# Optimization experiments

Hardware: AMD Instinct MI355X
Metric: run time of the kernel (lower is better)

Reference implementation:

```python
import jax, jax.numpy as jnp
import numpy as np

H = 4096      # hidden_size (Llama-7B)
I = 11008     # intermediate_size (Llama-7B)
T = 4096      # tokens = batch 2 * seq 2048


def setup_inputs() -> dict:
    key = jax.random.key(0)
    ks = jax.random.split(key, 10)
    # int8 activations in [-128, 127]
    x = jax.random.randint(ks[0], (T, H), -128, 128, dtype=jnp.int32).astype(jnp.int8)
    # int4 weights stored as int8 values in [-8, 7], layout [out, in]
    gate_w = jax.random.randint(ks[1], (I, H), -8, 8, dtype=jnp.int32).astype(jnp.int8)
    up_w   = jax.random.randint(ks[2], (I, H), -8, 8, dtype=jnp.int32).astype(jnp.int8)
    down_w = jax.random.randint(ks[3], (H, I), -8, 8, dtype=jnp.int32).astype(jnp.int8)
    # per-output-channel dequant scale (input_scale * weight_scale) and fp32 bias
    gate_alpha = jax.random.uniform(ks[4], (I,), jnp.float32, 1e-4, 3e-4)
    up_alpha   = jax.random.uniform(ks[5], (I,), jnp.float32, 1e-4, 3e-4)
    down_alpha = jax.random.uniform(ks[6], (H,), jnp.float32, 1e-4, 3e-4)
    gate_bias = jax.random.normal(ks[7], (I,), jnp.float32) * 0.01
    up_bias   = jax.random.normal(ks[8], (I,), jnp.float32) * 0.01
    down_bias = jax.random.normal(ks[9], (H,), jnp.float32) * 0.01
    down_input_scale = jnp.array(0.1, dtype=jnp.float32)
    return dict(x=x, gate_w=gate_w, up_w=up_w, down_w=down_w,
                gate_alpha=gate_alpha, gate_bias=gate_bias,
                up_alpha=up_alpha, up_bias=up_bias,
                down_alpha=down_alpha, down_bias=down_bias,
                down_input_scale=down_input_scale)


def _w4a8_linear(x_i8, w_i4, alpha, bias):
    # int8 act x int4 weight -> int32 accumulate, per-out-channel dequant, fp32 out
    acc = jnp.matmul(x_i8.astype(jnp.int32), w_i4.T.astype(jnp.int32))  # [T, out]
    return acc.astype(jnp.float32) * alpha + bias


def reference(x, gate_w, up_w, down_w, gate_alpha, gate_bias, up_alpha, up_bias,
              down_alpha, down_bias, down_input_scale):
    g = _w4a8_linear(x, gate_w, gate_alpha, gate_bias)          # [T, I] fp32
    u = _w4a8_linear(x, up_w, up_alpha, up_bias)                # [T, I] fp32
    h = jax.nn.silu(g) * u                                      # SwiGLU
    # requantize to int8 for down_proj input (values kept exact as fp32)
    hq = jnp.clip(jnp.round(h / down_input_scale), -128.0, 127.0)
    out = jnp.matmul(hq, down_w.T.astype(jnp.float32)) * down_alpha + down_bias
    return out
```

## Files before the change

kernel.cpp:

```cpp
#include <hip/hip_runtime.h>
#include <stdint.h>

#define H_DIM 4096
#define I_DIM 11008
#define T_DIM 4096

typedef int i32x4 __attribute__((ext_vector_type(4)));
typedef const void __attribute__((address_space(1))) gvoid_t;
typedef void __attribute__((address_space(3))) svoid_t;

__device__ __forceinline__ void gload_lds16(const void* gsrc, void* ldst) {
    __builtin_amdgcn_global_load_lds((gvoid_t*)gsrc, (svoid_t*)ldst, 16, 0, 0);
}
__device__ __forceinline__ void wait_vmcnt8() {
    asm volatile("s_waitcnt vmcnt(8)" ::: "memory");
}
__device__ __forceinline__ void wait_vmcnt0() {
    asm volatile("s_waitcnt vmcnt(0)" ::: "memory");
}
__device__ __forceinline__ void wait_lgkm0() {
    asm volatile("s_waitcnt lgkmcnt(0)" ::: "memory");
    __builtin_amdgcn_sched_barrier(0);
}
__device__ __forceinline__ void barrier_() {
    asm volatile("s_barrier" ::: "memory");
}

__device__ __forceinline__ uint32_t pack4(int4 v) {
    uint32_t r = (uint32_t)(uint8_t)v.x;
    r |= (uint32_t)(uint8_t)v.y << 8;
    r |= (uint32_t)(uint8_t)v.z << 16;
    r |= (uint32_t)(uint8_t)v.w << 24;
    return r;
}

__global__ void convert_kernel(const int* __restrict__ src, int8_t* __restrict__ dst,
                               int n4) {
    int idx = blockIdx.x * blockDim.x + threadIdx.x;
    int stride = gridDim.x * blockDim.x;
    for (int i = idx; i < n4; i += stride) {
        int4 v = ((const int4*)src)[i];
        ((uint32_t*)dst)[i] = pack4(v);
    }
}

__global__ void convert_frag_kernel(const int* __restrict__ src, int8_t* __restrict__ dst,
                                    int nslots, int kdiv16) {
    const int K = kdiv16 << 4;
    int idx = blockIdx.x * blockDim.x + threadIdx.x;
    int stride = gridDim.x * blockDim.x;
    for (int s = idx; s < nslots; s += stride) {
        const int n_lo = s & 15;
        const int srem = s >> 4;
        const int ks = srem % kdiv16;
        const int nb = srem / kdiv16;
        const int4* p = (const int4*)(src + (size_t)(nb * 16 + n_lo) * K + ks * 16);
        uint4 w;
        w.x = pack4(p[0]); w.y = pack4(p[1]); w.z = pack4(p[2]); w.w = pack4(p[3]);
        const size_t doff = ((size_t)nb * (kdiv16 >> 2) + (ks >> 2)) * 1024
                          + (size_t)(ks & 3) * 256 + (size_t)n_lo * 16;
        *(uint4*)(dst + doff) = w;
    }
}

#define MFMA_I8 __builtin_amdgcn_mfma_i32_16x16x64_i8

__global__ __launch_bounds__(512, 4)
void gateup_kernel(const int8_t* __restrict__ x8, const int8_t* __restrict__ gwf,
                   const int8_t* __restrict__ uwf,
                   const float* __restrict__ galpha, const float* __restrict__ gbias,
                   const float* __restrict__ ualpha, const float* __restrict__ ubias,
                   const float* __restrict__ scale_p, int8_t* __restrict__ hq)
{
    __shared__ __align__(16) int8_t smem_s[65536];

    const int bid = blockIdx.x;
    const int mt = bid & 31;
    const int nt = bid >> 5;
    const int m0 = mt << 7;
    const int n0 = nt << 7;

    const int tid  = threadIdx.x;
    const int lane = tid & 63;
    const int wid  = tid >> 6;
    const int isU  = wid >> 2;
    const int w4   = wid & 3;
    const int wr   = w4 >> 1;
    const int wc   = w4 & 1;
    const int lr   = lane & 15;
    const int rdsw = ((lane >> 4) ^ ((lr >> 1) & 3)) << 4;

    const int srow = tid >> 2;
    const int scol = ((tid & 3) ^ ((tid >> 3) & 3)) << 4;
    const int woff = wid << 10;

    const int8_t* As = x8 + (size_t)(m0 + srow) * H_DIM + scol;
    const int KB64 = H_DIM >> 6;
    const int8_t* Bsel = isU ? uwf : gwf;
    const int8_t* Bq = Bsel + ((size_t)((n0 >> 4) + wc * 4) * KB64) * 1024 + lane * 16;

    i32x4 acc[4][4];
#pragma unroll
    for (int mf = 0; mf < 4; ++mf)
#pragma unroll
        for (int nf = 0; nf < 4; ++nf) acc[mf][nf] = i32x4{0, 0, 0, 0};

    const int aro = (wr * 64 + lr) * 64 + rdsw;

#define STAGE_CH(b, ch) do { \
        _Pragma("unroll") for (int i_ = 0; i_ < 4; ++i_) \
            gload_lds16(As + (ch) * 256 + i_ * 64, \
                        smem_s + (b) * 32768 + i_ * 8192 + woff); \
    } while (0)

#define BLOAD(BF, tt) do { \
        _Pragma("unroll") for (int nf = 0; nf < 4; ++nf) \
            BF[nf] = *(const i32x4*)(Bq + ((size_t)nf * KB64 + (tt)) * 1024); \
    } while (0)

#define INNER(i_, BF, BFN, c_) do { \
        i32x4 af[4]; \
        _Pragma("unroll") for (int mf = 0; mf < 4; ++mf) \
            af[mf] = *(const i32x4*)(smem_s + ((c_) & 1) * 32768 + (i_) * 8192 \
                                     + aro + mf * 1024); \
        BLOAD(BFN, ((c_) * 4 + (i_) + 1) & (NKT - 1)); \
        __builtin_amdgcn_s_setprio(1); \
        _Pragma("unroll") for (int mf = 0; mf < 4; ++mf) \
        _Pragma("unroll") for (int nf = 0; nf < 4; ++nf) \
            acc[mf][nf] = MFMA_I8(af[mf], BF[nf], acc[mf][nf], 0, 0, 0); \
        __builtin_amdgcn_s_setprio(0); \
    } while (0)

    const int NKT = H_DIM / 64;
    const int NC  = NKT / 4;
    i32x4 bfA[4], bfB[4];
    STAGE_CH(0, 0);
    STAGE_CH(1, 1);
    BLOAD(bfA, 0);

    for (int c = 0; c < NC; ++c) {
        wait_vmcnt8();
        barrier_();
        INNER(0, bfA, bfB, c);
        INNER(1, bfB, bfA, c);
        INNER(2, bfA, bfB, c);
        INNER(3, bfB, bfA, c);
        wait_lgkm0();
        barrier_();
        STAGE_CH(c & 1, (c + 2) & (NC - 1));
    }
#undef INNER
#undef BLOAD
#undef STAGE_CH
    wait_vmcnt0();
    barrier_();

    const float scale = *scale_p;
#pragma unroll
    for (int h = 0; h < 2; ++h) {
        if (isU) {
#pragma unroll
            for (int mf = 0; mf < 4; ++mf)
#pragma unroll
                for (int q = 0; q < 2; ++q)
                    *(i32x4*)(smem_s + w4 * 8192 + mf * 2048 + q * 1024 + lane * 16)
                        = acc[mf][h * 2 + q];
        }
        barrier_();
        if (!isU) {
#pragma unroll
            for (int q = 0; q < 2; ++q) {
                const int nf = h * 2 + q;
                const int col = n0 + wc * 64 + nf * 16 + lr;
                const float gA = galpha[col], gB = gbias[col];
                const float uA = ualpha[col], uB = ubias[col];
#pragma unroll
                for (int mf = 0; mf < 4; ++mf) {
                    i32x4 uacc = *(const i32x4*)(smem_s + w4 * 8192 + mf * 2048
                                                 + q * 1024 + lane * 16);
                    const int row0 = m0 + wr * 64 + mf * 16 + (lane >> 4) * 4;
#pragma unroll
                    for (int j = 0; j < 4; ++j) {
                        float g = (float)acc[mf][nf][j] * gA + gB;
                        float u = (float)uacc[j] * uA + uB;
                        float s = 1.0f / (1.0f + __expf(-g));
                        float hh = g * s * u;
                        float qv = rintf(hh / scale);
                        qv = fminf(127.0f, fmaxf(-128.0f, qv));
                        hq[(size_t)(row0 + j) * I_DIM + col] = (int8_t)qv;
                    }
                }
            }
        }
        barrier_();
    }
}

__global__ __launch_bounds__(512, 4)
void down_kernel(const int8_t* __restrict__ hq, const int8_t* __restrict__ dwf,
                 const float* __restrict__ dalpha, const float* __restrict__ dbias,
                 float* __restrict__ out)
{
    __shared__ __align__(16) int8_t smem_d[65536];

    const int bid = blockIdx.x;
    const int mt = bid & 31;
    const int nt = bid >> 5;
    const int m0 = mt << 7;
    const int n0 = nt << 8;

    const int tid  = threadIdx.x;
    const int lane = tid & 63;
    const int wid  = tid >> 6;
    const int wr   = wid >> 2;
    const int wc   = wid & 3;
    const int lr   = lane & 15;
    const int rdsw = ((lane >> 4) ^ ((lr >> 1) & 3)) << 4;

    const int srow = tid >> 2;
    const int scol = ((tid & 3) ^ ((tid >> 3) & 3)) << 4;
    const int woff = wid << 10;

    const int8_t* Ap = hq + (size_t)(m0 + srow) * I_DIM + scol;
    const int KB64 = I_DIM >> 6;
    const int8_t* Bq = dwf + ((size_t)((n0 >> 4) + wc * 4) * KB64) * 1024 + lane * 16;

    i32x4 acc[4][4];
#pragma unroll
    for (int mf = 0; mf < 4; ++mf)
#pragma unroll
        for (int nf = 0; nf < 4; ++nf) acc[mf][nf] = i32x4{0, 0, 0, 0};

    const int aro = (wr * 64 + lr) * 64 + rdsw;

#define STAGE_CH(b, ch) do { \
        _Pragma("unroll") for (int i_ = 0; i_ < 4; ++i_) \
            gload_lds16(Ap + (size_t)(ch) * 256 + i_ * 64, \
                        smem_d + (b) * 32768 + i_ * 8192 + woff); \
    } while (0)

#define BLOAD(BF, tt) do { \
        _Pragma("unroll") for (int nf = 0; nf < 4; ++nf) \
            BF[nf] = *(const i32x4*)(Bq + ((size_t)nf * KB64 + (tt)) * 1024); \
    } while (0)

#define INNER(i_, BF, BFN, c_) do { \
        i32x4 af[4]; \
        _Pragma("unroll") for (int mf = 0; mf < 4; ++mf) \
            af[mf] = *(const i32x4*)(smem_d + ((c_) & 1) * 32768 + (i_) * 8192 \
                                     + aro + mf * 1024); \
        BLOAD(BFN, ((c_) * 4 + (i_) + 1) % NKT); \
        __builtin_amdgcn_s_setprio(1); \
        _Pragma("unroll") for (int mf = 0; mf < 4; ++mf) \
        _Pragma("unroll") for (int nf = 0; nf < 4; ++nf) \
            acc[mf][nf] = MFMA_I8(af[mf], BF[nf], acc[mf][nf], 0, 0, 0); \
        __builtin_amdgcn_s_setprio(0); \
    } while (0)

    const int NKT = I_DIM / 64;
    const int NC  = NKT / 4;
    i32x4 bfA[4], bfB[4];
    STAGE_CH(0, 0);
    STAGE_CH(1, 1);
    BLOAD(bfA, 0);

    for (int c = 0; c < NC; ++c) {
        wait_vmcnt8();
        barrier_();
        INNER(0, bfA, bfB, c);
        INNER(1, bfB, bfA, c);
        INNER(2, bfA, bfB, c);
        INNER(3, bfB, bfA, c);
        wait_lgkm0();
        barrier_();
        STAGE_CH(c & 1, (c + 2) % NC);
    }
#undef INNER
#undef BLOAD
#undef STAGE_CH
    wait_vmcnt0();

#pragma unroll
    for (int nf = 0; nf < 4; ++nf) {
        const int col = n0 + wc * 64 + nf * 16 + lr;
        const float dA = dalpha[col], dB = dbias[col];
#pragma unroll
        for (int mf = 0; mf < 4; ++mf) {
            const int row0 = m0 + wr * 64 + mf * 16 + (lane >> 4) * 4;
#pragma unroll
            for (int j = 0; j < 4; ++j) {
                out[(size_t)(row0 + j) * H_DIM + col] = (float)acc[mf][nf][j] * dA + dB;
            }
        }
    }
}

extern "C" void kernel_launch(void* const* d_in, const int* in_sizes, int n_in,
                              void* d_out, int out_size, void* d_ws, size_t ws_size,
                              hipStream_t stream) {
    const int* x32  = (const int*)d_in[0];
    const int* gw32 = (const int*)d_in[1];
    const int* uw32 = (const int*)d_in[2];
    const int* dw32 = (const int*)d_in[3];
    const float* ga = (const float*)d_in[4];
    const float* gb = (const float*)d_in[5];
    const float* ua = (const float*)d_in[6];
    const float* ub = (const float*)d_in[7];
    const float* da = (const float*)d_in[8];
    const float* db = (const float*)d_in[9];
    const float* sc = (const float*)d_in[10];
    float* out = (float*)d_out;

    const size_t SZ_X8 = (size_t)T_DIM * H_DIM;
    const size_t SZ_W  = (size_t)I_DIM * H_DIM;
    const size_t SZ_HQ = (size_t)T_DIM * I_DIM;

    int8_t* gwf = (int8_t*)d_ws;
    int8_t* uwf = gwf + SZ_W;
    int8_t* hq  = uwf + SZ_W;
    int8_t* x8  = hq + SZ_HQ;

    convert_kernel<<<dim3(2048), dim3(256), 0, stream>>>(x32, x8, (int)(SZ_X8 / 4));
    convert_frag_kernel<<<dim3(2048), dim3(256), 0, stream>>>(
        gw32, gwf, (int)(SZ_W / 16), H_DIM / 16);
    convert_frag_kernel<<<dim3(2048), dim3(256), 0, stream>>>(
        uw32, uwf, (int)(SZ_W / 16), H_DIM / 16);
    gateup_kernel<<<dim3(32 * 86), dim3(512), 0, stream>>>(
        x8, gwf, uwf, ga, gb, ua, ub, sc, hq);
    int8_t* dwf = gwf;
    convert_frag_kernel<<<dim3(2048), dim3(256), 0, stream>>>(
        dw32, dwf, (int)(SZ_W / 16), I_DIM / 16);
    down_kernel<<<dim3(32 * 16), dim3(512), 0, stream>>>(hq, dwf, da, db, out);
}
```

Before: 677.5 us.

## Reshape per-warp tiles to 128x32 so B fragments are loaded once per warp

Each warp's output tile changes from 64x64 (4x4 MFMA fragments) to a full-height 128x32 strip (8x2 fragments) in both the gate/up and down kernels. Every warp now reads all 128 A rows from LDS but loads only two B fragments directly from global memory, which halves per-warp global B traffic and removes the duplicate B loads between row-warps. The cost is double the LDS A reads per warp. The vmcnt wait threshold and the epilogue indexing are adjusted to match the new fragment layout.

```diff
diff --git a/kernel.cpp b/kernel.cpp
--- a/kernel.cpp
+++ b/kernel.cpp
@@ -12,8 +12,8 @@
 __device__ __forceinline__ void gload_lds16(const void* gsrc, void* ldst) {
     __builtin_amdgcn_global_load_lds((gvoid_t*)gsrc, (svoid_t*)ldst, 16, 0, 0);
 }
-__device__ __forceinline__ void wait_vmcnt8() {
-    asm volatile("s_waitcnt vmcnt(8)" ::: "memory");
+__device__ __forceinline__ void wait_vmcnt6() {
+    asm volatile("s_waitcnt vmcnt(6)" ::: "memory");
 }
 __device__ __forceinline__ void wait_vmcnt0() {
     asm volatile("s_waitcnt vmcnt(0)" ::: "memory");
@@ -85,8 +85,6 @@
     const int wid  = tid >> 6;
     const int isU  = wid >> 2;
     const int w4   = wid & 3;
-    const int wr   = w4 >> 1;
-    const int wc   = w4 & 1;
     const int lr   = lane & 15;
     const int rdsw = ((lane >> 4) ^ ((lr >> 1) & 3)) << 4;
 
@@ -97,15 +95,15 @@
     const int8_t* As = x8 + (size_t)(m0 + srow) * H_DIM + scol;
     const int KB64 = H_DIM >> 6;
     const int8_t* Bsel = isU ? uwf : gwf;
-    const int8_t* Bq = Bsel + ((size_t)((n0 >> 4) + wc * 4) * KB64) * 1024 + lane * 16;
-
-    i32x4 acc[4][4];
-#pragma unroll
-    for (int mf = 0; mf < 4; ++mf)
-#pragma unroll
-        for (int nf = 0; nf < 4; ++nf) acc[mf][nf] = i32x4{0, 0, 0, 0};
-
-    const int aro = (wr * 64 + lr) * 64 + rdsw;
+    const int8_t* Bq = Bsel + ((size_t)((n0 >> 4) + w4 * 2) * KB64) * 1024 + lane * 16;
+
+    i32x4 acc[8][2];
+#pragma unroll
+    for (int mf = 0; mf < 8; ++mf)
+#pragma unroll
+        for (int nf = 0; nf < 2; ++nf) acc[mf][nf] = i32x4{0, 0, 0, 0};
+
+    const int aro = lr * 64 + rdsw;
 
 #define STAGE_CH(b, ch) do { \
         _Pragma("unroll") for (int i_ = 0; i_ < 4; ++i_) \
@@ -114,32 +112,32 @@
     } while (0)
 
 #define BLOAD(BF, tt) do { \
-        _Pragma("unroll") for (int nf = 0; nf < 4; ++nf) \
+        _Pragma("unroll") for (int nf = 0; nf < 2; ++nf) \
             BF[nf] = *(const i32x4*)(Bq + ((size_t)nf * KB64 + (tt)) * 1024); \
     } while (0)
 
 #define INNER(i_, BF, BFN, c_) do { \
-        i32x4 af[4]; \
-        _Pragma("unroll") for (int mf = 0; mf < 4; ++mf) \
+        i32x4 af[8]; \
+        _Pragma("unroll") for (int mf = 0; mf < 8; ++mf) \
             af[mf] = *(const i32x4*)(smem_s + ((c_) & 1) * 32768 + (i_) * 8192 \
                                      + aro + mf * 1024); \
         BLOAD(BFN, ((c_) * 4 + (i_) + 1) & (NKT - 1)); \
         __builtin_amdgcn_s_setprio(1); \
-        _Pragma("unroll") for (int mf = 0; mf < 4; ++mf) \
-        _Pragma("unroll") for (int nf = 0; nf < 4; ++nf) \
+        _Pragma("unroll") for (int mf = 0; mf < 8; ++mf) \
+        _Pragma("unroll") for (int nf = 0; nf < 2; ++nf) \
             acc[mf][nf] = MFMA_I8(af[mf], BF[nf], acc[mf][nf], 0, 0, 0); \
         __builtin_amdgcn_s_setprio(0); \
     } while (0)
 
     const int NKT = H_DIM / 64;
     const int NC  = NKT / 4;
-    i32x4 bfA[4], bfB[4];
+    i32x4 bfA[2], bfB[2];
     STAGE_CH(0, 0);
     STAGE_CH(1, 1);
     BLOAD(bfA, 0);
 
     for (int c = 0; c < NC; ++c) {
-        wait_vmcnt8();
+        wait_vmcnt6();
         barrier_();
         INNER(0, bfA, bfB, c);
         INNER(1, bfB, bfA, c);
@@ -160,28 +158,27 @@
     for (int h = 0; h < 2; ++h) {
         if (isU) {
 #pragma unroll
-            for (int mf = 0; mf < 4; ++mf)
-#pragma unroll
-                for (int q = 0; q < 2; ++q)
-                    *(i32x4*)(smem_s + w4 * 8192 + mf * 2048 + q * 1024 + lane * 16)
-                        = acc[mf][h * 2 + q];
+            for (int mq = 0; mq < 4; ++mq)
+#pragma unroll
+                for (int nf = 0; nf < 2; ++nf)
+                    *(i32x4*)(smem_s + w4 * 8192 + mq * 2048 + nf * 1024 + lane * 16)
+                        = acc[h * 4 + mq][nf];
         }
         barrier_();
         if (!isU) {
 #pragma unroll
-            for (int q = 0; q < 2; ++q) {
-                const int nf = h * 2 + q;
-                const int col = n0 + wc * 64 + nf * 16 + lr;
+            for (int nf = 0; nf < 2; ++nf) {
+                const int col = n0 + w4 * 32 + nf * 16 + lr;
                 const float gA = galpha[col], gB = gbias[col];
                 const float uA = ualpha[col], uB = ubias[col];
 #pragma unroll
-                for (int mf = 0; mf < 4; ++mf) {
-                    i32x4 uacc = *(const i32x4*)(smem_s + w4 * 8192 + mf * 2048
-                                                 + q * 1024 + lane * 16);
-                    const int row0 = m0 + wr * 64 + mf * 16 + (lane >> 4) * 4;
+                for (int mq = 0; mq < 4; ++mq) {
+                    i32x4 uacc = *(const i32x4*)(smem_s + w4 * 8192 + mq * 2048
+                                                 + nf * 1024 + lane * 16);
+                    const int row0 = m0 + (h * 4 + mq) * 16 + (lane >> 4) * 4;
 #pragma unroll
                     for (int j = 0; j < 4; ++j) {
-                        float g = (float)acc[mf][nf][j] * gA + gB;
+                        float g = (float)acc[h * 4 + mq][nf][j] * gA + gB;
                         float u = (float)uacc[j] * uA + uB;
                         float s = 1.0f / (1.0f + __expf(-g));
                         float hh = g * s * u;
@@ -212,8 +209,6 @@
     const int tid  = threadIdx.x;
     const int lane = tid & 63;
     const int wid  = tid >> 6;
-    const int wr   = wid >> 2;
-    const int wc   = wid & 3;
     const int lr   = lane & 15;
     const int rdsw = ((lane >> 4) ^ ((lr >> 1) & 3)) << 4;
 
@@ -223,15 +218,15 @@
 
     const int8_t* Ap = hq + (size_t)(m0 + srow) * I_DIM + scol;
     const int KB64 = I_DIM >> 6;
-    const int8_t* Bq = dwf + ((size_t)((n0 >> 4) + wc * 4) * KB64) * 1024 + lane * 16;
-
-    i32x4 acc[4][4];
-#pragma unroll
-    for (int mf = 0; mf < 4; ++mf)
-#pragma unroll
-        for (int nf = 0; nf < 4; ++nf) acc[mf][nf] = i32x4{0, 0, 0, 0};
-
-    const int aro = (wr * 64 + lr) * 64 + rdsw;
+    const int8_t* Bq = dwf + ((size_t)((n0 >> 4) + wid * 2) * KB64) * 1024 + lane * 16;
+
+    i32x4 acc[8][2];
+#pragma unroll
+    for (int mf = 0; mf < 8; ++mf)
+#pragma unroll
+        for (int nf = 0; nf < 2; ++nf) acc[mf][nf] = i32x4{0, 0, 0, 0};
+
+    const int aro = lr * 64 + rdsw;
 
 #define STAGE_CH(b, ch) do { \
         _Pragma("unroll") for (int i_ = 0; i_ < 4; ++i_) \
@@ -240,32 +235,32 @@
     } while (0)
 
 #define BLOAD(BF, tt) do { \
-        _Pragma("unroll") for (int nf = 0; nf < 4; ++nf) \
+        _Pragma("unroll") for (int nf = 0; nf < 2; ++nf) \
             BF[nf] = *(const i32x4*)(Bq + ((size_t)nf * KB64 + (tt)) * 1024); \
     } while (0)
 
 #define INNER(i_, BF, BFN, c_) do { \
-        i32x4 af[4]; \
-        _Pragma("unroll") for (int mf = 0; mf < 4; ++mf) \
+        i32x4 af[8]; \
+        _Pragma("unroll") for (int mf = 0; mf < 8; ++mf) \
             af[mf] = *(const i32x4*)(smem_d + ((c_) & 1) * 32768 + (i_) * 8192 \
                                      + aro + mf * 1024); \
         BLOAD(BFN, ((c_) * 4 + (i_) + 1) % NKT); \
         __builtin_amdgcn_s_setprio(1); \
-        _Pragma("unroll") for (int mf = 0; mf < 4; ++mf) \
-        _Pragma("unroll") for (int nf = 0; nf < 4; ++nf) \
+        _Pragma("unroll") for (int mf = 0; mf < 8; ++mf) \
+        _Pragma("unroll") for (int nf = 0; nf < 2; ++nf) \
             acc[mf][nf] = MFMA_I8(af[mf], BF[nf], acc[mf][nf], 0, 0, 0); \
         __builtin_amdgcn_s_setprio(0); \
     } while (0)
 
     const int NKT = I_DIM / 64;
     const int NC  = NKT / 4;
-    i32x4 bfA[4], bfB[4];
+    i32x4 bfA[2], bfB[2];
     STAGE_CH(0, 0);
     STAGE_CH(1, 1);
     BLOAD(bfA, 0);
 
     for (int c = 0; c < NC; ++c) {
-        wait_vmcnt8();
+        wait_vmcnt6();
         barrier_();
         INNER(0, bfA, bfB, c);
         INNER(1, bfB, bfA, c);
@@ -281,12 +276,12 @@
     wait_vmcnt0();
 
 #pragma unroll
-    for (int nf = 0; nf < 4; ++nf) {
-        const int col = n0 + wc * 64 + nf * 16 + lr;
+    for (int nf = 0; nf < 2; ++nf) {
+        const int col = n0 + wid * 32 + nf * 16 + lr;
         const float dA = dalpha[col], dB = dbias[col];
 #pragma unroll
-        for (int mf = 0; mf < 4; ++mf) {
-            const int row0 = m0 + wr * 64 + mf * 16 + (lane >> 4) * 4;
+        for (int mf = 0; mf < 8; ++mf) {
+            const int row0 = m0 + mf * 16 + (lane >> 4) * 4;
 #pragma unroll
             for (int j = 0; j < 4; ++j) {
                 out[(size_t)(row0 + j) * H_DIM + col] = (float)acc[mf][nf][j] * dA + dB;
```

Result: faster. 639.6 us (-5.6%).

## Halve block threads and double per-warp tile in gate-up and down GEMMs

Applied to the files above, without the earlier changes.

Both GEMM kernels drop from 512 to 256 threads per block, so each wave computes a larger output tile. In gateup, every wave now holds both gate and up accumulators, which removes the LDS exchange and barriers in the SwiGLU epilogue and reuses each A fragment for two MFMAs. In down, each wave covers 8 column fragments instead of 4. This doubles accumulator registers per wave and lowers the number of waves per CU, trading occupancy and latency hiding for more register-level data reuse.

```diff
diff --git a/kernel.cpp b/kernel.cpp
--- a/kernel.cpp
+++ b/kernel.cpp
@@ -12,8 +12,8 @@
 __device__ __forceinline__ void gload_lds16(const void* gsrc, void* ldst) {
     __builtin_amdgcn_global_load_lds((gvoid_t*)gsrc, (svoid_t*)ldst, 16, 0, 0);
 }
-__device__ __forceinline__ void wait_vmcnt8() {
-    asm volatile("s_waitcnt vmcnt(8)" ::: "memory");
+__device__ __forceinline__ void wait_vmcnt16() {
+    asm volatile("s_waitcnt vmcnt(16)" ::: "memory");
 }
 __device__ __forceinline__ void wait_vmcnt0() {
     asm volatile("s_waitcnt vmcnt(0)" ::: "memory");
@@ -65,7 +65,7 @@
 
 #define MFMA_I8 __builtin_amdgcn_mfma_i32_16x16x64_i8
 
-__global__ __launch_bounds__(512, 4)
+__global__ __launch_bounds__(256, 2)
 void gateup_kernel(const int8_t* __restrict__ x8, const int8_t* __restrict__ gwf,
                    const int8_t* __restrict__ uwf,
                    const float* __restrict__ galpha, const float* __restrict__ gbias,
@@ -83,10 +83,8 @@
     const int tid  = threadIdx.x;
     const int lane = tid & 63;
     const int wid  = tid >> 6;
-    const int isU  = wid >> 2;
-    const int w4   = wid & 3;
-    const int wr   = w4 >> 1;
-    const int wc   = w4 & 1;
+    const int wrr  = wid >> 1;
+    const int wcc  = wid & 1;
     const int lr   = lane & 15;
     const int rdsw = ((lane >> 4) ^ ((lr >> 1) & 3)) << 4;
 
@@ -96,55 +94,65 @@
 
     const int8_t* As = x8 + (size_t)(m0 + srow) * H_DIM + scol;
     const int KB64 = H_DIM >> 6;
-    const int8_t* Bsel = isU ? uwf : gwf;
-    const int8_t* Bq = Bsel + ((size_t)((n0 >> 4) + wc * 4) * KB64) * 1024 + lane * 16;
-
-    i32x4 acc[4][4];
+    const int8_t* BqG = gwf + ((size_t)((n0 >> 4) + wcc * 4) * KB64) * 1024 + lane * 16;
+    const int8_t* BqU = uwf + ((size_t)((n0 >> 4) + wcc * 4) * KB64) * 1024 + lane * 16;
+
+    i32x4 accg[4][4], accu[4][4];
 #pragma unroll
     for (int mf = 0; mf < 4; ++mf)
 #pragma unroll
-        for (int nf = 0; nf < 4; ++nf) acc[mf][nf] = i32x4{0, 0, 0, 0};
-
-    const int aro = (wr * 64 + lr) * 64 + rdsw;
+        for (int nf = 0; nf < 4; ++nf) {
+            accg[mf][nf] = i32x4{0, 0, 0, 0};
+            accu[mf][nf] = i32x4{0, 0, 0, 0};
+        }
+
+    const int aro = (wrr * 64 + lr) * 64 + rdsw;
 
 #define STAGE_CH(b, ch) do { \
-        _Pragma("unroll") for (int i_ = 0; i_ < 4; ++i_) \
+        _Pragma("unroll") for (int i_ = 0; i_ < 4; ++i_) { \
             gload_lds16(As + (ch) * 256 + i_ * 64, \
                         smem_s + (b) * 32768 + i_ * 8192 + woff); \
-    } while (0)
-
-#define BLOAD(BF, tt) do { \
-        _Pragma("unroll") for (int nf = 0; nf < 4; ++nf) \
-            BF[nf] = *(const i32x4*)(Bq + ((size_t)nf * KB64 + (tt)) * 1024); \
-    } while (0)
-
-#define INNER(i_, BF, BFN, c_) do { \
+            gload_lds16(As + (size_t)64 * H_DIM + (ch) * 256 + i_ * 64, \
+                        smem_s + (b) * 32768 + i_ * 8192 + 4096 + woff); \
+        } \
+    } while (0)
+
+#define BLOAD(BG, BU, tt) do { \
+        _Pragma("unroll") for (int nf = 0; nf < 4; ++nf) { \
+            BG[nf] = *(const i32x4*)(BqG + ((size_t)nf * KB64 + (tt)) * 1024); \
+            BU[nf] = *(const i32x4*)(BqU + ((size_t)nf * KB64 + (tt)) * 1024); \
+        } \
+    } while (0)
+
+#define INNER(i_, BG, BU, BGN, BUN, c_) do { \
         i32x4 af[4]; \
         _Pragma("unroll") for (int mf = 0; mf < 4; ++mf) \
             af[mf] = *(const i32x4*)(smem_s + ((c_) & 1) * 32768 + (i_) * 8192 \
                                      + aro + mf * 1024); \
-        BLOAD(BFN, ((c_) * 4 + (i_) + 1) & (NKT - 1)); \
+        BLOAD(BGN, BUN, ((c_) * 4 + (i_) + 1) & (NKT - 1)); \
         __builtin_amdgcn_s_setprio(1); \
         _Pragma("unroll") for (int mf = 0; mf < 4; ++mf) \
-        _Pragma("unroll") for (int nf = 0; nf < 4; ++nf) \
-            acc[mf][nf] = MFMA_I8(af[mf], BF[nf], acc[mf][nf], 0, 0, 0); \
+        _Pragma("unroll") for (int nf = 0; nf < 4; ++nf) { \
+            accg[mf][nf] = MFMA_I8(af[mf], BG[nf], accg[mf][nf], 0, 0, 0); \
+            accu[mf][nf] = MFMA_I8(af[mf], BU[nf], accu[mf][nf], 0, 0, 0); \
+        } \
         __builtin_amdgcn_s_setprio(0); \
     } while (0)
 
     const int NKT = H_DIM / 64;
     const int NC  = NKT / 4;
-    i32x4 bfA[4], bfB[4];
+    i32x4 bgA[4], buA[4], bgB[4], buB[4];
     STAGE_CH(0, 0);
     STAGE_CH(1, 1);
-    BLOAD(bfA, 0);
+    BLOAD(bgA, buA, 0);
 
     for (int c = 0; c < NC; ++c) {
-        wait_vmcnt8();
+        wait_vmcnt16();
         barrier_();
-        INNER(0, bfA, bfB, c);
-        INNER(1, bfB, bfA, c);
-        INNER(2, bfA, bfB, c);
-        INNER(3, bfB, bfA, c);
+        INNER(0, bgA, buA, bgB, buB, c);
+        INNER(1, bgB, buB, bgA, buA, c);
+        INNER(2, bgA, buA, bgB, buB, c);
+        INNER(3, bgB, buB, bgA, buA, c);
         wait_lgkm0();
         barrier_();
         STAGE_CH(c & 1, (c + 2) & (NC - 1));
@@ -153,50 +161,31 @@
 #undef BLOAD
 #undef STAGE_CH
     wait_vmcnt0();
-    barrier_();
 
     const float scale = *scale_p;
 #pragma unroll
-    for (int h = 0; h < 2; ++h) {
-        if (isU) {
-#pragma unroll
-            for (int mf = 0; mf < 4; ++mf)
-#pragma unroll
-                for (int q = 0; q < 2; ++q)
-                    *(i32x4*)(smem_s + w4 * 8192 + mf * 2048 + q * 1024 + lane * 16)
-                        = acc[mf][h * 2 + q];
-        }
-        barrier_();
-        if (!isU) {
-#pragma unroll
-            for (int q = 0; q < 2; ++q) {
-                const int nf = h * 2 + q;
-                const int col = n0 + wc * 64 + nf * 16 + lr;
-                const float gA = galpha[col], gB = gbias[col];
-                const float uA = ualpha[col], uB = ubias[col];
-#pragma unroll
-                for (int mf = 0; mf < 4; ++mf) {
-                    i32x4 uacc = *(const i32x4*)(smem_s + w4 * 8192 + mf * 2048
-                                                 + q * 1024 + lane * 16);
-                    const int row0 = m0 + wr * 64 + mf * 16 + (lane >> 4) * 4;
-#pragma unroll
-                    for (int j = 0; j < 4; ++j) {
-                        float g = (float)acc[mf][nf][j] * gA + gB;
-                        float u = (float)uacc[j] * uA + uB;
-                        float s = 1.0f / (1.0f + __expf(-g));
-                        float hh = g * s * u;
-                        float qv = rintf(hh / scale);
-                        qv = fminf(127.0f, fmaxf(-128.0f, qv));
-                        hq[(size_t)(row0 + j) * I_DIM + col] = (int8_t)qv;
-                    }
-                }
+    for (int nf = 0; nf < 4; ++nf) {
+        const int col = n0 + wcc * 64 + nf * 16 + lr;
+        const float gA = galpha[col], gB = gbias[col];
+        const float uA = ualpha[col], uB = ubias[col];
+#pragma unroll
+        for (int mf = 0; mf < 4; ++mf) {
+            const int row0 = m0 + wrr * 64 + mf * 16 + (lane >> 4) * 4;
+#pragma unroll
+            for (int j = 0; j < 4; ++j) {
+                float g = (float)accg[mf][nf][j] * gA + gB;
+                float u = (float)accu[mf][nf][j] * uA + uB;
+                float s = 1.0f / (1.0f + __expf(-g));
+                float hh = g * s * u;
+                float qv = rintf(hh / scale);
+                qv = fminf(127.0f, fmaxf(-128.0f, qv));
+                hq[(size_t)(row0 + j) * I_DIM + col] = (int8_t)qv;
             }
         }
-        barrier_();
-    }
-}
-
-__global__ __launch_bounds__(512, 4)
+    }
+}
+
+__global__ __launch_bounds__(256, 2)
 void down_kernel(const int8_t* __restrict__ hq, const int8_t* __restrict__ dwf,
                  const float* __restrict__ dalpha, const float* __restrict__ dbias,
                  float* __restrict__ out)
@@ -212,8 +201,8 @@
     const int tid  = threadIdx.x;
     const int lane = tid & 63;
     const int wid  = tid >> 6;
-    const int wr   = wid >> 2;
-    const int wc   = wid & 3;
+    const int wrr  = wid >> 1;
+    const int wcc  = wid & 1;
     const int lr   = lane & 15;
     const int rdsw = ((lane >> 4) ^ ((lr >> 1) & 3)) << 4;
 
@@ -223,24 +212,27 @@
 
     const int8_t* Ap = hq + (size_t)(m0 + srow) * I_DIM + scol;
     const int KB64 = I_DIM >> 6;
-    const int8_t* Bq = dwf + ((size_t)((n0 >> 4) + wc * 4) * KB64) * 1024 + lane * 16;
-
-    i32x4 acc[4][4];
+    const int8_t* Bq = dwf + ((size_t)((n0 >> 4) + wcc * 8) * KB64) * 1024 + lane * 16;
+
+    i32x4 acc[4][8];
 #pragma unroll
     for (int mf = 0; mf < 4; ++mf)
 #pragma unroll
-        for (int nf = 0; nf < 4; ++nf) acc[mf][nf] = i32x4{0, 0, 0, 0};
-
-    const int aro = (wr * 64 + lr) * 64 + rdsw;
+        for (int nf = 0; nf < 8; ++nf) acc[mf][nf] = i32x4{0, 0, 0, 0};
+
+    const int aro = (wrr * 64 + lr) * 64 + rdsw;
 
 #define STAGE_CH(b, ch) do { \
-        _Pragma("unroll") for (int i_ = 0; i_ < 4; ++i_) \
+        _Pragma("unroll") for (int i_ = 0; i_ < 4; ++i_) { \
             gload_lds16(Ap + (size_t)(ch) * 256 + i_ * 64, \
                         smem_d + (b) * 32768 + i_ * 8192 + woff); \
+            gload_lds16(Ap + (size_t)64 * I_DIM + (size_t)(ch) * 256 + i_ * 64, \
+                        smem_d + (b) * 32768 + i_ * 8192 + 4096 + woff); \
+        } \
     } while (0)
 
 #define BLOAD(BF, tt) do { \
-        _Pragma("unroll") for (int nf = 0; nf < 4; ++nf) \
+        _Pragma("unroll") for (int nf = 0; nf < 8; ++nf) \
             BF[nf] = *(const i32x4*)(Bq + ((size_t)nf * KB64 + (tt)) * 1024); \
     } while (0)
 
@@ -252,20 +244,20 @@
         BLOAD(BFN, ((c_) * 4 + (i_) + 1) % NKT); \
         __builtin_amdgcn_s_setprio(1); \
         _Pragma("unroll") for (int mf = 0; mf < 4; ++mf) \
-        _Pragma("unroll") for (int nf = 0; nf < 4; ++nf) \
+        _Pragma("unroll") for (int nf = 0; nf < 8; ++nf) \
             acc[mf][nf] = MFMA_I8(af[mf], BF[nf], acc[mf][nf], 0, 0, 0); \
         __builtin_amdgcn_s_setprio(0); \
     } while (0)
 
     const int NKT = I_DIM / 64;
     const int NC  = NKT / 4;
-    i32x4 bfA[4], bfB[4];
+    i32x4 bfA[8], bfB[8];
     STAGE_CH(0, 0);
     STAGE_CH(1, 1);
     BLOAD(bfA, 0);
 
     for (int c = 0; c < NC; ++c) {
-        wait_vmcnt8();
+        wait_vmcnt16();
         barrier_();
         INNER(0, bfA, bfB, c);
         INNER(1, bfB, bfA, c);
@@ -281,12 +273,12 @@
     wait_vmcnt0();
 
 #pragma unroll
-    for (int nf = 0; nf < 4; ++nf) {
-        const int col = n0 + wc * 64 + nf * 16 + lr;
+    for (int nf = 0; nf < 8; ++nf) {
+        const int col = n0 + wcc * 128 + nf * 16 + lr;
         const float dA = dalpha[col], dB = dbias[col];
 #pragma unroll
         for (int mf = 0; mf < 4; ++mf) {
-            const int row0 = m0 + wr * 64 + mf * 16 + (lane >> 4) * 4;
+            const int row0 = m0 + wrr * 64 + mf * 16 + (lane >> 4) * 4;
 #pragma unroll
             for (int j = 0; j < 4; ++j) {
                 out[(size_t)(row0 + j) * H_DIM + col] = (float)acc[mf][nf][j] * dA + dB;
@@ -325,10 +317,10 @@
         gw32, gwf, (int)(SZ_W / 16), H_DIM / 16);
     convert_frag_kernel<<<dim3(2048), dim3(256), 0, stream>>>(
         uw32, uwf, (int)(SZ_W / 16), H_DIM / 16);
-    gateup_kernel<<<dim3(32 * 86), dim3(512), 0, stream>>>(
+    gateup_kernel<<<dim3(32 * 86), dim3(256), 0, stream>>>(
         x8, gwf, uwf, ga, gb, ua, ub, sc, hq);
     int8_t* dwf = gwf;
     convert_frag_kernel<<<dim3(2048), dim3(256), 0, stream>>>(
         dw32, dwf, (int)(SZ_W / 16), I_DIM / 16);
-    down_kernel<<<dim3(32 * 16), dim3(512), 0, stream>>>(hq, dwf, da, db, out);
-}
+    down_kernel<<<dim3(32 * 16), dim3(256), 0, stream>>>(hq, dwf, da, db, out);
+}
```

Result: no change. 671.9 us (-0.8%).
